# Performance work log

Measured on AMD Instinct MI355X. Metric: run time of the kernel, lower is better.

## Reference

```python
import jax, jax.numpy as jnp
import numpy as np

B, L, D, H = 32, 1024, 512, 8
G = 64 + 1          # groups + cls token -> number of query/target tokens
K = 16              # num_per_group (top-k)
DH = D // H


def setup_inputs() -> dict:
    key = jax.random.key(0)
    ks = jax.random.split(key, 12)
    s = D ** -0.5
    return {
        "x": jax.random.normal(ks[0], (B, L, D), jnp.float32),
        "Wq": jax.random.normal(ks[1], (D, D), jnp.float32) * s,
        "bq": jnp.zeros((D,), jnp.float32),
        "Wk": jax.random.normal(ks[2], (D, D), jnp.float32) * s,
        "bk": jnp.zeros((D,), jnp.float32),
        "Wv": jax.random.normal(ks[3], (D, D), jnp.float32) * s,
        "bv": jnp.zeros((D,), jnp.float32),
        "Wo": jax.random.normal(ks[4], (D, D), jnp.float32) * s,
        "bo": jnp.zeros((D,), jnp.float32),
        "target": jax.random.uniform(ks[5], (G, D), jnp.float32),      # torch.rand init
        "conv_w": jax.random.normal(ks[6], (G, K), jnp.float32) * (K ** -0.5),  # Conv1d(G*K->G, groups=G, k=1)
        "conv_b": jax.random.normal(ks[7], (G,), jnp.float32) * 0.01,
    }


def reference(x, Wq, bq, Wk, bk, Wv, bv, Wo, bo, target, conv_w, conv_b):
    b = x.shape[0]
    # sum_or_prod == 'prod': log(relu(x)+1) input transform
    x = jnp.log(jax.nn.relu(x) + 1.0)
    # cluster=True, target_mode != 'mix': queries come from learned target tokens
    tgt = jnp.broadcast_to(target[None], (b, G, D))
    q = (tgt @ Wq + bq).reshape(b, G, H, DH).transpose(0, 2, 1, 3)   # [b,h,G,dh]
    k = (x @ Wk + bk).reshape(b, L, H, DH).transpose(0, 2, 1, 3)     # [b,h,L,dh]
    v = (x @ Wv + bv).reshape(b, L, H, DH).transpose(0, 2, 1, 3)     # [b,h,L,dh]
    # scale = (dim/heads) ** -0.5 = dh ** -0.5
    scores = jnp.einsum('bhqd,bhkd->bhqk', q, k) * (DH ** -0.5)      # [b,h,G,L]
    attn = jax.nn.softmax(scores, axis=-1)
    # top-k selection over attention weights, gather corresponding values
    _, idx = jax.lax.top_k(attn, K)                                  # [b,h,G,K]
    xx = jnp.take_along_axis(v[:, :, None, :, :], idx[..., None], axis=3)  # [b,h,G,K,dh]
    # grouped 1x1 conv combine: per-query weighted sum over the K gathered values
    y = jnp.einsum('bhqkc,qk->bhqc', xx, conv_w) + conv_b[None, None, :, None]
    # 'prod' post: global min-max normalize then exp
    mn, mx = y.min(), y.max()
    y = jnp.exp((y - mn) / (mx - mn))
    out = y.transpose(0, 2, 1, 3).reshape(b, G, D)                   # b n (h d)
    return out @ Wo + bo
```

## Files before the change

### kernel.cpp

```cpp
#include <hip/hip_runtime.h>
#include <math.h>

#define B_  32
#define L_  1024
#define D_  512
#define H_  8
#define G_  65
#define K_  16
#define DH_ 64
#define HG_  (H_ * G_)
#define HGP2_ 640
#define BL_  (B_ * L_)
#define NROW_ (B_ * H_ * G_)
#define M_OUT_ (B_ * G_)

typedef _Float16 f16x8 __attribute__((ext_vector_type(8)));
typedef float f32x4 __attribute__((ext_vector_type(4)));

__device__ __forceinline__ unsigned int f2s(float f) {
  unsigned int u = __float_as_uint(f);
  return (u & 0x80000000u) ? ~u : (u | 0x80000000u);
}
__device__ __forceinline__ float s2f(unsigned int u) {
  return __uint_as_float((u & 0x80000000u) ? (u & 0x7FFFFFFFu) : ~u);
}
__device__ __forceinline__ void split16(float v, _Float16* h, _Float16* l) {
  _Float16 h0 = (_Float16)v;
  float hf = (float)h0;
  if (fabsf(v) < 6.103515625e-05f) { h0 = (_Float16)0.f; hf = 0.f; }
  *h = h0;
  *l = (_Float16)((v - hf) * 4096.0f);
}
__device__ __forceinline__ void gload16(const void* g, void* l) {
  __builtin_amdgcn_global_load_lds(
      (const __attribute__((address_space(1))) unsigned int*)g,
      (__attribute__((address_space(3))) unsigned int*)l, 16, 0, 0);
}
__device__ __forceinline__ size_t pk_idx(int row, int c) {
  return (((size_t)(row >> 4) * 16 + (c >> 5)) << 9) +
         ((((c & 31) >> 3) << 4) + (row & 15)) * 8 + (c & 7);
}

__global__ void transform_split_kernel(const float* __restrict__ x,
                                       _Float16* __restrict__ th16,
                                       _Float16* __restrict__ tl16, int n4) {
  int i = blockIdx.x * blockDim.x + threadIdx.x;
  int stride = gridDim.x * blockDim.x;
  const float4* x4 = (const float4*)x;
  for (; i < n4; i += stride) {
    float4 a = x4[i];
    float t[4];
    t[0] = logf(fmaxf(a.x, 0.f) + 1.f);
    t[1] = logf(fmaxf(a.y, 0.f) + 1.f);
    t[2] = logf(fmaxf(a.z, 0.f) + 1.f);
    t[3] = logf(fmaxf(a.w, 0.f) + 1.f);
    _Float16 h[4], l[4];
#pragma unroll
    for (int j = 0; j < 4; ++j) split16(t[j], &h[j], &l[j]);
    *(ushort4*)&th16[i * 4] = *(ushort4*)h;
    *(ushort4*)&tl16[i * 4] = *(ushort4*)l;
  }
}

__global__ __launch_bounds__(256) void wprep_kernel(const float* __restrict__ Wv,
                                                    const float* __restrict__ Wo,
                                                    _Float16* __restrict__ wvtp,
                                                    _Float16* __restrict__ wotp) {
  int n = blockIdx.x;
  for (int k = threadIdx.x; k < 512; k += 256) {
    size_t o = pk_idx(n, k);
    wvtp[o] = (_Float16)Wv[(size_t)k * 512 + n];
    wotp[o] = (_Float16)Wo[(size_t)k * 512 + n];
  }
}

__global__ __launch_bounds__(256) void qproj_kernel(const float* __restrict__ target,
                                                    const float* __restrict__ Wq,
                                                    const float* __restrict__ bq,
                                                    float* __restrict__ q) {
  int g = blockIdx.x;
  int d = blockIdx.y * 256 + threadIdx.x;
  __shared__ float ts[512];
  for (int i = threadIdx.x; i < 512; i += 256) ts[i] = target[g * 512 + i];
  __syncthreads();
  float acc = bq[d];
  for (int c = 0; c < 512; ++c) acc += ts[c] * Wq[c * 512 + d];
  q[g * 512 + d] = acc;
}

__global__ __launch_bounds__(256) void p_kernel(const float* __restrict__ q,
                                                const float* __restrict__ Wk,
                                                _Float16* __restrict__ pph,
                                                _Float16* __restrict__ ppl) {
  int hg = blockIdx.x;
  int tid = threadIdx.x;
  if (hg >= HG_) {
    for (int c = tid; c < 512; c += 256) {
      size_t o = pk_idx(hg, c);
      pph[o] = (_Float16)0.f;
      ppl[o] = (_Float16)0.f;
    }
    return;
  }
  int h = hg / G_, g = hg % G_;
  __shared__ float4 qs[16];
  if (tid < 16) qs[tid] = *(const float4*)&q[g * 512 + h * 64 + tid * 4];
  __syncthreads();
#pragma unroll
  for (int cc = 0; cc < 2; ++cc) {
    int c = cc * 256 + tid;
    const float4* wr = (const float4*)&Wk[(size_t)c * 512 + h * 64];
    float acc = 0.f;
#pragma unroll
    for (int jj = 0; jj < 16; ++jj) {
      float4 wv = wr[jj];
      float4 qv = qs[jj];
      acc += wv.x * qv.x + wv.y * qv.y + wv.z * qv.z + wv.w * qv.w;
    }
    _Float16 hh, ll;
    split16(acc, &hh, &ll);
    size_t o = pk_idx(hg, c);
    pph[o] = hh;
    ppl[o] = ll;
  }
}

__global__ __launch_bounds__(512, 4) void scores_gemm_kernel(
    const _Float16* __restrict__ th16, const _Float16* __restrict__ tl16,
    const _Float16* __restrict__ pph, const _Float16* __restrict__ ppl,
    float* __restrict__ scores) {
  __shared__ char lds[65536];
  const int w = blockIdx.x;
  const int xcd = w & 7;
  const int j = w >> 3;
  const int n0 = (xcd * 32 + j / 5) * 128;
  const int mt = j % 5;
  const int m0 = mt * 128;
  const int mt0 = mt * 8;
  const int tid = threadIdx.x;
  const int lane = tid & 63;
  const int wv = tid >> 6;
  const int wm = wv >> 1;
  const int wn = wv & 1;
  const int l16 = lane & 15;
  const int lg = lane >> 4;

  f32x4 acc0[2][4], acc1[2][4];
#pragma unroll
  for (int i = 0; i < 2; ++i)
#pragma unroll
    for (int jj = 0; jj < 4; ++jj) { acc0[i][jj] = (f32x4)(0.f); acc1[i][jj] = (f32x4)(0.f); }

  const int st_row = tid >> 2;
  const int st_s   = tid & 3;

#define STAGE_SC(buf, ks)                                                      \
  {                                                                            \
    size_t tsrc = (size_t)(n0 + st_row) * 512 + (ks) * 32 +                    \
                  ((st_s ^ (st_row & 3)) << 3);                                \
    char* tb = lds + (buf) * 32768 + tid * 16;                                 \
    gload16(th16 + tsrc, tb);                                                  \
    gload16(tl16 + tsrc, tb + 8192);                                           \
    _Pragma("unroll")                                                          \
    for (int i = 0; i < 2; ++i) {                                              \
      int f = wv * 2 + i;                          \
      int fm = f >= 8 ? f - 8 : f;                                             \
      const _Float16* sp = (f >= 8) ? ppl : pph;                               \
      size_t src = (((size_t)(mt0 + fm) * 16 + (ks)) << 9) + lane * 8;         \
      gload16(sp + src, lds + (buf) * 32768 + 16384 + f * 1024);               \
    }                                                                          \
  }

  STAGE_SC(0, 0);
  __syncthreads();

  for (int ks = 0; ks < 16; ++ks) {
    const int cur = ks & 1;
    if (ks < 15) STAGE_SC(cur ^ 1, ks + 1);
    const char* abase = lds + cur * 32768 + 16384;
    f16x8 Ah[2], Al[2];
#pragma unroll
    for (int fm = 0; fm < 2; ++fm) {
      int f = wm * 2 + fm;
      Ah[fm] = *(const f16x8*)(abase + f * 1024 + lane * 16);
      Al[fm] = *(const f16x8*)(abase + (8 + f) * 1024 + lane * 16);
    }
#pragma unroll
    for (int fn = 0; fn < 4; ++fn) {
      int r = wn * 64 + fn * 16 + l16;
      int addr = cur * 32768 + r * 64 + ((lg ^ (r & 3)) << 4);
      f16x8 Bh = *(const f16x8*)(lds + addr);
      f16x8 Bl = *(const f16x8*)(lds + addr + 8192);
#pragma unroll
      for (int fm = 0; fm < 2; ++fm) {
        acc0[fm][fn] = __builtin_amdgcn_mfma_f32_16x16x32_f16(Ah[fm], Bh, acc0[fm][fn], 0, 0, 0);
        acc1[fm][fn] = __builtin_amdgcn_mfma_f32_16x16x32_f16(Ah[fm], Bl, acc1[fm][fn], 0, 0, 0);
        acc1[fm][fn] = __builtin_amdgcn_mfma_f32_16x16x32_f16(Al[fm], Bh, acc1[fm][fn], 0, 0, 0);
      }
    }
    __syncthreads();
  }
#undef STAGE_SC

#pragma unroll
  for (int fm = 0; fm < 2; ++fm) {
    int hg0 = m0 + (wm * 2 + fm) * 16 + (lg << 2);
#pragma unroll
    for (int fn = 0; fn < 4; ++fn) {
      int col = n0 + wn * 64 + fn * 16 + l16;
#pragma unroll
      for (int r = 0; r < 4; ++r) {
        int row = hg0 + r;
        if (row < HG_)
          scores[(size_t)row * BL_ + col] =
              acc0[fm][fn][r] + acc1[fm][fn][r] * 0.000244140625f;
      }
    }
  }
}

__global__ __launch_bounds__(256, 2) void vgemm_kernel(
    const _Float16* __restrict__ th16, const _Float16* __restrict__ wvtp,
    const float* __restrict__ bv, _Float16* __restrict__ vout) {
  __shared__ char lds[16384];
  const int tid = threadIdx.x;
  const int lane = tid & 63;
  const int wid = tid >> 6;
  const int wave_m = wid >> 1;
  const int wave_n = wid & 1;
  const int m0 = blockIdx.x * 128;
  const int n0 = blockIdx.y * 128;

  f32x4 acc[4][4];
#pragma unroll
  for (int i = 0; i < 4; ++i)
#pragma unroll
    for (int j = 0; j < 4; ++j) acc[i][j] = (f32x4)(0.f);

  for (int k0 = 0; k0 < 512; k0 += 64) {
#pragma unroll
    for (int it = 0; it < 4; ++it) {
      int row = it * 32 + (tid >> 3);
      int j = tid & 7;
      size_t src = (size_t)(m0 + row) * 512 + k0 + ((j ^ (row & 7)) << 3);
      gload16(th16 + src, lds + it * 4096 + wid * 1024);
    }
    __syncthreads();
#pragma unroll
    for (int kh = 0; kh < 2; ++kh) {
      f16x8 Bv[4];
#pragma unroll
      for (int fn = 0; fn < 4; ++fn) {
        size_t bo = (((size_t)(n0 >> 4) + wave_n * 4 + fn) * 16 +
                     (k0 >> 5) + kh) * 512 + lane * 8;
        Bv[fn] = *(const f16x8*)(wvtp + bo);
      }
#pragma unroll
      for (int fm = 0; fm < 4; ++fm) {
        int r = wave_m * 64 + fm * 16 + (lane & 15);
        int jl = kh * 4 + (lane >> 4);
        f16x8 Af = *(const f16x8*)(lds + r * 128 + ((jl ^ (r & 7)) << 4));
#pragma unroll
        for (int fn = 0; fn < 4; ++fn)
          acc[fm][fn] = __builtin_amdgcn_mfma_f32_16x16x32_f16(Af, Bv[fn], acc[fm][fn], 0, 0, 0);
      }
    }
    __syncthreads();
  }
#pragma unroll
  for (int fm = 0; fm < 4; ++fm) {
#pragma unroll
    for (int fn = 0; fn < 4; ++fn) {
      int col = n0 + wave_n * 64 + fn * 16 + (lane & 15);
      float bvv = bv[col];
#pragma unroll
      for (int r = 0; r < 4; ++r) {
        int row = m0 + wave_m * 64 + fm * 16 + ((lane >> 4) << 2) + r;
        vout[(size_t)row * 512 + col] = (_Float16)(acc[fm][fn][r] + bvv);
      }
    }
  }
}

__global__ __launch_bounds__(256) void topk_conv_kernel(const float* __restrict__ scores,
                                                        const _Float16* __restrict__ vbuf,
                                                        const float* __restrict__ conv_w,
                                                        const float* __restrict__ conv_b,
                                                        float* __restrict__ y,
                                                        float2* __restrict__ wmm) {
  int row = blockIdx.x * 4 + (threadIdx.x >> 6);
  int lane = threadIdx.x & 63;
  int g = row % G_;
  int bh = row / G_;
  int b = bh >> 3, h = bh & 7;
  const float* srow = scores + (size_t)(h * G_ + g) * BL_ + b * 1024;

  float s[16];
#pragma unroll
  for (int j = 0; j < 16; ++j) s[j] = srow[j * 64 + lane];

  int sel[16];
#pragma unroll
  for (int r = 0; r < 16; ++r) {
    float bs = s[0];
    int bl = lane;
#pragma unroll
    for (int j = 1; j < 16; ++j) {
      bool t = s[j] > bs;
      bs = t ? s[j] : bs;
      bl = t ? j * 64 + lane : bl;
    }
#pragma unroll
    for (int off = 32; off > 0; off >>= 1) {
      float os = __shfl_xor(bs, off);
      int ol = __shfl_xor(bl, off);
      bool take = (os > bs) || (os == bs && ol < bl);
      bs = take ? os : bs;
      bl = take ? ol : bl;
    }
#pragma unroll
    for (int j = 0; j < 16; ++j)
      if (bl == j * 64 + lane) s[j] = -INFINITY;
    sel[r] = __builtin_amdgcn_readfirstlane(bl);
  }

  const _Float16* vrow = vbuf + (size_t)b * 1024 * 512 + h * 64 + lane;
  float acc = conv_b[g];
#pragma unroll
  for (int r = 0; r < 16; ++r)
    acc += conv_w[g * 16 + r] * (float)vrow[(size_t)sel[r] * 512];

  y[(size_t)row * 64 + lane] = acc;

  float mn = acc, mx = acc;
#pragma unroll
  for (int off = 32; off > 0; off >>= 1) {
    float o = __shfl_xor(mn, off); mn = fminf(mn, o);
    float p = __shfl_xor(mx, off); mx = fmaxf(mx, p);
  }
  if (lane == 0) wmm[row] = make_float2(mn, mx);
}

__global__ __launch_bounds__(256) void minmax_reduce_kernel(const float2* __restrict__ wmm,
                                                            unsigned int* __restrict__ minmax) {
  int i = blockIdx.x * 256 + threadIdx.x;
  float2 v = wmm[i];
  float mn = v.x, mx = v.y;
#pragma unroll
  for (int off = 32; off > 0; off >>= 1) {
    float o = __shfl_xor(mn, off); mn = fminf(mn, o);
    float p = __shfl_xor(mx, off); mx = fmaxf(mx, p);
  }
  __shared__ float smn[4], smx[4];
  int lane = threadIdx.x & 63, wid = threadIdx.x >> 6;
  if (lane == 0) { smn[wid] = mn; smx[wid] = mx; }
  __syncthreads();
  if (threadIdx.x == 0) {
    mn = fminf(fminf(smn[0], smn[1]), fminf(smn[2], smn[3]));
    mx = fmaxf(fmaxf(smx[0], smx[1]), fmaxf(smx[2], smx[3]));
    atomicMin(&minmax[0], f2s(mn));
    atomicMax(&minmax[1], f2s(mx));
  }
}

__global__ void zprep_kernel(const float* __restrict__ y,
                             const unsigned int* __restrict__ minmax,
                             _Float16* __restrict__ z16) {
  int i = blockIdx.x * 256 + threadIdx.x;
  float mn = s2f(minmax[0]);
  float mx = s2f(minmax[1]);
  float inv = 1.f / (mx - mn);
  int c = i & 63;
  int t = i >> 6;
  int g = t % G_;
  int bh = t / G_;
  int b = bh >> 3, h = bh & 7;
  z16[(size_t)(b * G_ + g) * 512 + h * 64 + c] = (_Float16)expf((y[i] - mn) * inv);
}

__global__ __launch_bounds__(256, 2) void out_gemm_kernel(
    const _Float16* __restrict__ z16, const _Float16* __restrict__ wotp,
    const float* __restrict__ bo, float* __restrict__ out) {
  __shared__ char lds[16384];
  const int tid = threadIdx.x;
  const int lane = tid & 63;
  const int wid = tid >> 6;
  const int wave_m = wid >> 1;
  const int wave_n = wid & 1;
  const int m0 = blockIdx.x * 128;
  const int n0 = blockIdx.y * 128;

  f32x4 acc[4][4];
#pragma unroll
  for (int i = 0; i < 4; ++i)
#pragma unroll
    for (int j = 0; j < 4; ++j) acc[i][j] = (f32x4)(0.f);

  for (int k0 = 0; k0 < 512; k0 += 64) {
#pragma unroll
    for (int it = 0; it < 4; ++it) {
      int row = it * 32 + (tid >> 3);
      int grow = m0 + row;
      if (grow > M_OUT_ - 1) grow = M_OUT_ - 1;
      int j = tid & 7;
      size_t src = (size_t)grow * 512 + k0 + ((j ^ (row & 7)) << 3);
      gload16(z16 + src, lds + it * 4096 + wid * 1024);
    }
    __syncthreads();
#pragma unroll
    for (int kh = 0; kh < 2; ++kh) {
      f16x8 Bw[4];
#pragma unroll
      for (int fn = 0; fn < 4; ++fn) {
        size_t bo_off = (((size_t)(n0 >> 4) + wave_n * 4 + fn) * 16 +
                         (k0 >> 5) + kh) * 512 + lane * 8;
        Bw[fn] = *(const f16x8*)(wotp + bo_off);
      }
#pragma unroll
      for (int fm = 0; fm < 4; ++fm) {
        int r = wave_m * 64 + fm * 16 + (lane & 15);
        int jl = kh * 4 + (lane >> 4);
        f16x8 Af = *(const f16x8*)(lds + r * 128 + ((jl ^ (r & 7)) << 4));
#pragma unroll
        for (int fn = 0; fn < 4; ++fn)
          acc[fm][fn] = __builtin_amdgcn_mfma_f32_16x16x32_f16(Af, Bw[fn], acc[fm][fn], 0, 0, 0);
      }
    }
    __syncthreads();
  }
#pragma unroll
  for (int fm = 0; fm < 4; ++fm) {
#pragma unroll
    for (int fn = 0; fn < 4; ++fn) {
      int col = n0 + wave_n * 64 + fn * 16 + (lane & 15);
      float bov = bo[col];
#pragma unroll
      for (int r = 0; r < 4; ++r) {
        int row = m0 + wave_m * 64 + fm * 16 + ((lane >> 4) << 2) + r;
        if (row < M_OUT_)
          out[(size_t)row * 512 + col] = acc[fm][fn][r] + bov;
      }
    }
  }
}

extern "C" void kernel_launch(void* const* d_in, const int* in_sizes, int n_in,
                              void* d_out, int out_size, void* d_ws, size_t ws_size,
                              hipStream_t stream) {
  const float* x      = (const float*)d_in[0];
  const float* Wq     = (const float*)d_in[1];
  const float* bq     = (const float*)d_in[2];
  const float* Wk     = (const float*)d_in[3];
  const float* bk     = (const float*)d_in[4];
  const float* Wv     = (const float*)d_in[5];
  const float* bv     = (const float*)d_in[6];
  const float* Wo     = (const float*)d_in[7];
  const float* bo     = (const float*)d_in[8];
  const float* target = (const float*)d_in[9];
  const float* conv_w = (const float*)d_in[10];
  const float* conv_b = (const float*)d_in[11];
  float* out = (float*)d_out;
  (void)bk;

  char* ws = (char*)d_ws;
  _Float16*      th16  = (_Float16*)(ws);
  _Float16*      tl16  = (_Float16*)(ws + 33554432);
  _Float16*      vbf   = (_Float16*)(ws + 67108864);
  float*         sc    = (float*)(ws + 100663296);
  _Float16*      pph   = (_Float16*)(ws + 168820736);
  _Float16*      ppl   = (_Float16*)(ws + 169476096);
  _Float16*      wvtp  = (_Float16*)(ws + 170131456);
  _Float16*      wotp  = (_Float16*)(ws + 170655744);
  float*         qb    = (float*)(ws + 171180032);
  float*         yb    = (float*)(ws + 171313152);
  _Float16*      z16   = (_Float16*)(ws + 175572992);
  unsigned int*  mm    = (unsigned int*)(ws + 177702912);
  float2*        wmm   = (float2*)(ws + 177702928);

  hipMemsetAsync(mm, 0xFF, 4, stream);
  hipMemsetAsync((char*)mm + 4, 0x00, 4, stream);

  transform_split_kernel<<<2048, 256, 0, stream>>>(x, th16, tl16, B_ * L_ * D_ / 4);
  wprep_kernel<<<512, 256, 0, stream>>>(Wv, Wo, wvtp, wotp);
  qproj_kernel<<<dim3(G_, 2), 256, 0, stream>>>(target, Wq, bq, qb);
  p_kernel<<<HGP2_, 256, 0, stream>>>(qb, Wk, pph, ppl);
  scores_gemm_kernel<<<1280, 512, 0, stream>>>(th16, tl16, pph, ppl, sc);
  vgemm_kernel<<<dim3(256, 4), 256, 0, stream>>>(th16, wvtp, bv, vbf);
  topk_conv_kernel<<<NROW_ / 4, 256, 0, stream>>>(sc, vbf, conv_w, conv_b, yb, wmm);
  minmax_reduce_kernel<<<NROW_ / 256, 256, 0, stream>>>(wmm, mm);
  zprep_kernel<<<B_ * H_ * G_ * DH_ / 256, 256, 0, stream>>>(yb, mm, z16);
  out_gemm_kernel<<<dim3(17, 4), 256, 0, stream>>>(z16, wotp, bo, out);
}
```

Measured before the change: 241.0 us.

## Merge scores GEMM and V GEMM into one heterogeneous launch

Combines the scores GEMM and the value projection GEMM into one kernel that branches on block index. The first 1280 blocks compute scores and the remaining 512 compute V, with V retiled to 128x256 tiles over 512 threads. This removes one launch and the tail gap between the two dependent-free GEMMs so they can overlap on the GPU. In exchange the V blocks now run under the scores kernel's 64KB LDS and 512-thread launch bounds, which may lower their occupancy and raise register pressure.

```diff
diff --git a/kernel.cpp b/kernel.cpp
--- a/kernel.cpp
+++ b/kernel.cpp
@@ -125,158 +125,155 @@
   }
 }
 
-__global__ __launch_bounds__(512, 4) void scores_gemm_kernel(
+__global__ __launch_bounds__(512, 4) void fused_gemms_kernel(
     const _Float16* __restrict__ th16, const _Float16* __restrict__ tl16,
     const _Float16* __restrict__ pph, const _Float16* __restrict__ ppl,
-    float* __restrict__ scores) {
+    const _Float16* __restrict__ wvtp, const float* __restrict__ bv,
+    float* __restrict__ scores, _Float16* __restrict__ vout) {
   __shared__ char lds[65536];
-  const int w = blockIdx.x;
-  const int xcd = w & 7;
-  const int j = w >> 3;
-  const int n0 = (xcd * 32 + j / 5) * 128;
-  const int mt = j % 5;
-  const int m0 = mt * 128;
-  const int mt0 = mt * 8;
   const int tid = threadIdx.x;
   const int lane = tid & 63;
   const int wv = tid >> 6;
-  const int wm = wv >> 1;
-  const int wn = wv & 1;
   const int l16 = lane & 15;
   const int lg = lane >> 4;
 
-  f32x4 acc0[2][4], acc1[2][4];
-#pragma unroll
-  for (int i = 0; i < 2; ++i)
-#pragma unroll
-    for (int jj = 0; jj < 4; ++jj) { acc0[i][jj] = (f32x4)(0.f); acc1[i][jj] = (f32x4)(0.f); }
-
-  const int st_row = tid >> 2;
-  const int st_s   = tid & 3;
+  if (blockIdx.x < 1280) {
+    const int w = blockIdx.x;
+    const int xcd = w & 7;
+    const int j = w >> 3;
+    const int n0 = (xcd * 32 + j / 5) * 128;
+    const int mt = j % 5;
+    const int m0 = mt * 128;
+    const int mt0 = mt * 8;
+    const int wm = wv >> 1;
+    const int wn = wv & 1;
+
+    f32x4 acc0[2][4], acc1[2][4];
+#pragma unroll
+    for (int i = 0; i < 2; ++i)
+#pragma unroll
+      for (int jj = 0; jj < 4; ++jj) { acc0[i][jj] = (f32x4)(0.f); acc1[i][jj] = (f32x4)(0.f); }
+
+    const int st_row = tid >> 2;
+    const int st_s   = tid & 3;
 
 #define STAGE_SC(buf, ks)                                                      \
-  {                                                                            \
-    size_t tsrc = (size_t)(n0 + st_row) * 512 + (ks) * 32 +                    \
-                  ((st_s ^ (st_row & 3)) << 3);                                \
-    char* tb = lds + (buf) * 32768 + tid * 16;                                 \
-    gload16(th16 + tsrc, tb);                                                  \
-    gload16(tl16 + tsrc, tb + 8192);                                           \
-    _Pragma("unroll")                                                          \
-    for (int i = 0; i < 2; ++i) {                                              \
-      int f = wv * 2 + i;                          \
-      int fm = f >= 8 ? f - 8 : f;                                             \
-      const _Float16* sp = (f >= 8) ? ppl : pph;                               \
-      size_t src = (((size_t)(mt0 + fm) * 16 + (ks)) << 9) + lane * 8;         \
-      gload16(sp + src, lds + (buf) * 32768 + 16384 + f * 1024);               \
-    }                                                                          \
-  }
-
-  STAGE_SC(0, 0);
-  __syncthreads();
-
-  for (int ks = 0; ks < 16; ++ks) {
-    const int cur = ks & 1;
-    if (ks < 15) STAGE_SC(cur ^ 1, ks + 1);
-    const char* abase = lds + cur * 32768 + 16384;
-    f16x8 Ah[2], Al[2];
+    {                                                                          \
+      size_t tsrc = (size_t)(n0 + st_row) * 512 + (ks) * 32 +                  \
+                    ((st_s ^ (st_row & 3)) << 3);                              \
+      char* tb = lds + (buf) * 32768 + tid * 16;                               \
+      gload16(th16 + tsrc, tb);                                                \
+      gload16(tl16 + tsrc, tb + 8192);                                         \
+      _Pragma("unroll")                                                        \
+      for (int i = 0; i < 2; ++i) {                                            \
+        int f = wv * 2 + i;                                                    \
+        int fm = f >= 8 ? f - 8 : f;                                           \
+        const _Float16* sp = (f >= 8) ? ppl : pph;                             \
+        size_t src = (((size_t)(mt0 + fm) * 16 + (ks)) << 9) + lane * 8;       \
+        gload16(sp + src, lds + (buf) * 32768 + 16384 + f * 1024);             \
+      }                                                                        \
+    }
+
+    STAGE_SC(0, 0);
+    __syncthreads();
+
+    for (int ks = 0; ks < 16; ++ks) {
+      const int cur = ks & 1;
+      if (ks < 15) STAGE_SC(cur ^ 1, ks + 1);
+      const char* abase = lds + cur * 32768 + 16384;
+      f16x8 Ah[2], Al[2];
+#pragma unroll
+      for (int fm = 0; fm < 2; ++fm) {
+        int f = wm * 2 + fm;
+        Ah[fm] = *(const f16x8*)(abase + f * 1024 + lane * 16);
+        Al[fm] = *(const f16x8*)(abase + (8 + f) * 1024 + lane * 16);
+      }
+#pragma unroll
+      for (int fn = 0; fn < 4; ++fn) {
+        int r = wn * 64 + fn * 16 + l16;
+        int addr = cur * 32768 + r * 64 + ((lg ^ (r & 3)) << 4);
+        f16x8 Bh = *(const f16x8*)(lds + addr);
+        f16x8 Bl = *(const f16x8*)(lds + addr + 8192);
+#pragma unroll
+        for (int fm = 0; fm < 2; ++fm) {
+          acc0[fm][fn] = __builtin_amdgcn_mfma_f32_16x16x32_f16(Ah[fm], Bh, acc0[fm][fn], 0, 0, 0);
+          acc1[fm][fn] = __builtin_amdgcn_mfma_f32_16x16x32_f16(Ah[fm], Bl, acc1[fm][fn], 0, 0, 0);
+          acc1[fm][fn] = __builtin_amdgcn_mfma_f32_16x16x32_f16(Al[fm], Bh, acc1[fm][fn], 0, 0, 0);
+        }
+      }
+      __syncthreads();
+    }
+#undef STAGE_SC
+
 #pragma unroll
     for (int fm = 0; fm < 2; ++fm) {
-      int f = wm * 2 + fm;
-      Ah[fm] = *(const f16x8*)(abase + f * 1024 + lane * 16);
-      Al[fm] = *(const f16x8*)(abase + (8 + f) * 1024 + lane * 16);
-    }
-#pragma unroll
-    for (int fn = 0; fn < 4; ++fn) {
-      int r = wn * 64 + fn * 16 + l16;
-      int addr = cur * 32768 + r * 64 + ((lg ^ (r & 3)) << 4);
-      f16x8 Bh = *(const f16x8*)(lds + addr);
-      f16x8 Bl = *(const f16x8*)(lds + addr + 8192);
-#pragma unroll
-      for (int fm = 0; fm < 2; ++fm) {
-        acc0[fm][fn] = __builtin_amdgcn_mfma_f32_16x16x32_f16(Ah[fm], Bh, acc0[fm][fn], 0, 0, 0);
-        acc1[fm][fn] = __builtin_amdgcn_mfma_f32_16x16x32_f16(Ah[fm], Bl, acc1[fm][fn], 0, 0, 0);
-        acc1[fm][fn] = __builtin_amdgcn_mfma_f32_16x16x32_f16(Al[fm], Bh, acc1[fm][fn], 0, 0, 0);
-      }
-    }
-    __syncthreads();
-  }
-#undef STAGE_SC
-
-#pragma unroll
-  for (int fm = 0; fm < 2; ++fm) {
-    int hg0 = m0 + (wm * 2 + fm) * 16 + (lg << 2);
-#pragma unroll
-    for (int fn = 0; fn < 4; ++fn) {
-      int col = n0 + wn * 64 + fn * 16 + l16;
-#pragma unroll
-      for (int r = 0; r < 4; ++r) {
-        int row = hg0 + r;
-        if (row < HG_)
-          scores[(size_t)row * BL_ + col] =
-              acc0[fm][fn][r] + acc1[fm][fn][r] * 0.000244140625f;
-      }
-    }
-  }
-}
-
-__global__ __launch_bounds__(256, 2) void vgemm_kernel(
-    const _Float16* __restrict__ th16, const _Float16* __restrict__ wvtp,
-    const float* __restrict__ bv, _Float16* __restrict__ vout) {
-  __shared__ char lds[16384];
-  const int tid = threadIdx.x;
-  const int lane = tid & 63;
-  const int wid = tid >> 6;
-  const int wave_m = wid >> 1;
-  const int wave_n = wid & 1;
-  const int m0 = blockIdx.x * 128;
-  const int n0 = blockIdx.y * 128;
-
-  f32x4 acc[4][4];
-#pragma unroll
-  for (int i = 0; i < 4; ++i)
-#pragma unroll
-    for (int j = 0; j < 4; ++j) acc[i][j] = (f32x4)(0.f);
-
-  for (int k0 = 0; k0 < 512; k0 += 64) {
-#pragma unroll
-    for (int it = 0; it < 4; ++it) {
-      int row = it * 32 + (tid >> 3);
-      int j = tid & 7;
-      size_t src = (size_t)(m0 + row) * 512 + k0 + ((j ^ (row & 7)) << 3);
-      gload16(th16 + src, lds + it * 4096 + wid * 1024);
-    }
-    __syncthreads();
-#pragma unroll
-    for (int kh = 0; kh < 2; ++kh) {
-      f16x8 Bv[4];
+      int hg0 = m0 + (wm * 2 + fm) * 16 + (lg << 2);
 #pragma unroll
       for (int fn = 0; fn < 4; ++fn) {
-        size_t bo = (((size_t)(n0 >> 4) + wave_n * 4 + fn) * 16 +
-                     (k0 >> 5) + kh) * 512 + lane * 8;
-        Bv[fn] = *(const f16x8*)(wvtp + bo);
-      }
-#pragma unroll
-      for (int fm = 0; fm < 4; ++fm) {
-        int r = wave_m * 64 + fm * 16 + (lane & 15);
-        int jl = kh * 4 + (lane >> 4);
-        f16x8 Af = *(const f16x8*)(lds + r * 128 + ((jl ^ (r & 7)) << 4));
-#pragma unroll
-        for (int fn = 0; fn < 4; ++fn)
-          acc[fm][fn] = __builtin_amdgcn_mfma_f32_16x16x32_f16(Af, Bv[fn], acc[fm][fn], 0, 0, 0);
-      }
-    }
-    __syncthreads();
-  }
-#pragma unroll
-  for (int fm = 0; fm < 4; ++fm) {
-#pragma unroll
-    for (int fn = 0; fn < 4; ++fn) {
-      int col = n0 + wave_n * 64 + fn * 16 + (lane & 15);
-      float bvv = bv[col];
-#pragma unroll
-      for (int r = 0; r < 4; ++r) {
-        int row = m0 + wave_m * 64 + fm * 16 + ((lane >> 4) << 2) + r;
-        vout[(size_t)row * 512 + col] = (_Float16)(acc[fm][fn][r] + bvv);
+        int col = n0 + wn * 64 + fn * 16 + l16;
+#pragma unroll
+        for (int r = 0; r < 4; ++r) {
+          int row = hg0 + r;
+          if (row < HG_)
+            scores[(size_t)row * BL_ + col] =
+                acc0[fm][fn][r] + acc1[fm][fn][r] * 0.000244140625f;
+        }
+      }
+    }
+  } else {
+    const int vb = blockIdx.x - 1280;
+    const int m0 = (vb & 255) * 128;
+    const int nh = vb >> 8;
+    const int wm = wv & 1;
+    const int wn = wv >> 1;
+
+    f32x4 acc[4][4];
+#pragma unroll
+    for (int i = 0; i < 4; ++i)
+#pragma unroll
+      for (int jj = 0; jj < 4; ++jj) acc[i][jj] = (f32x4)(0.f);
+
+    for (int k0 = 0; k0 < 512; k0 += 64) {
+#pragma unroll
+      for (int it = 0; it < 2; ++it) {
+        int row = it * 64 + (tid >> 3);
+        int j8 = tid & 7;
+        size_t src = (size_t)(m0 + row) * 512 + k0 + ((j8 ^ (row & 7)) << 3);
+        gload16(th16 + src, lds + it * 8192 + tid * 16);
+      }
+      __syncthreads();
+#pragma unroll
+      for (int kh = 0; kh < 2; ++kh) {
+        f16x8 Bv[4];
+#pragma unroll
+        for (int fn = 0; fn < 4; ++fn) {
+          size_t bo = (((size_t)(nh * 16 + wn * 4 + fn)) * 16 +
+                       (k0 >> 5) + kh) * 512 + lane * 8;
+          Bv[fn] = *(const f16x8*)(wvtp + bo);
+        }
+#pragma unroll
+        for (int fm = 0; fm < 4; ++fm) {
+          int r = wm * 64 + fm * 16 + l16;
+          int jl = kh * 4 + lg;
+          f16x8 Af = *(const f16x8*)(lds + r * 128 + ((jl ^ (r & 7)) << 4));
+#pragma unroll
+          for (int fn = 0; fn < 4; ++fn)
+            acc[fm][fn] = __builtin_amdgcn_mfma_f32_16x16x32_f16(Af, Bv[fn], acc[fm][fn], 0, 0, 0);
+        }
+      }
+      __syncthreads();
+    }
+#pragma unroll
+    for (int fm = 0; fm < 4; ++fm) {
+#pragma unroll
+      for (int fn = 0; fn < 4; ++fn) {
+        int col = nh * 256 + wn * 64 + fn * 16 + l16;
+        float bvv = bv[col];
+#pragma unroll
+        for (int r = 0; r < 4; ++r) {
+          int row = m0 + wm * 64 + fm * 16 + (lg << 2) + r;
+          vout[(size_t)row * 512 + col] = (_Float16)(acc[fm][fn][r] + bvv);
+        }
       }
     }
   }
@@ -484,8 +481,7 @@
   wprep_kernel<<<512, 256, 0, stream>>>(Wv, Wo, wvtp, wotp);
   qproj_kernel<<<dim3(G_, 2), 256, 0, stream>>>(target, Wq, bq, qb);
   p_kernel<<<HGP2_, 256, 0, stream>>>(qb, Wk, pph, ppl);
-  scores_gemm_kernel<<<1280, 512, 0, stream>>>(th16, tl16, pph, ppl, sc);
-  vgemm_kernel<<<dim3(256, 4), 256, 0, stream>>>(th16, wvtp, bv, vbf);
+  fused_gemms_kernel<<<1792, 512, 0, stream>>>(th16, tl16, pph, ppl, wvtp, bv, sc, vbf);
   topk_conv_kernel<<<NROW_ / 4, 256, 0, stream>>>(sc, vbf, conv_w, conv_b, yb, wmm);
   minmax_reduce_kernel<<<NROW_ / 256, 256, 0, stream>>>(wmm, mm);
   zprep_kernel<<<B_ * H_ * G_ * DH_ / 256, 256, 0, stream>>>(yb, mm, z16);
```

After: 236.0 us, median of 2. 1.02x faster.
